# Kernel optimization log

Measured on AMD Instinct MI355X. Metric: run time of the kernel, lower is better.

Reference implementation:

```python
import jax, jax.numpy as jnp
import numpy as np

WINDOW = 60
DEPTH = 3
HIDDEN = 256
LN_EPS = 1e-5


def _lyndon_indices(d):
    # Lyndon words over alphabet {0..d-1}, lengths 2 and 3, lexicographic order
    # (signatory mode='words' extracts expanded-logsig coefficients at Lyndon words).
    i2 = np.array([(i, j) for i in range(d) for j in range(d) if (i, j) < (j, i)], dtype=np.int32)
    i3 = np.array([(i, j, k) for i in range(d) for j in range(d) for k in range(d)
                   if (i, j, k) < (j, k, i) and (i, j, k) < (k, i, j)], dtype=np.int32)
    return i2, i3


def _logsig_features(x):
    # x: [b, s, c] -> logsignature of time-augmented sliding windows: [b*s, sig_channels]
    b, s, c = x.shape
    d = c + 1
    # replicate-padded sliding windows via clipped gather (matches F.pad replicate + unfold)
    pos = jnp.clip(jnp.arange(s)[:, None] + jnp.arange(WINDOW)[None, :] - (WINDOW - 1), 0, s - 1)
    windows = x[:, pos, :]                                   # [b, s, W, c]
    t = jnp.linspace(0.0, 1.0, WINDOW, dtype=x.dtype)        # time augmentation channel
    t_b = jnp.broadcast_to(t[None, None, :, None], (b, s, WINDOW, 1))
    aug = jnp.concatenate([t_b, windows], axis=-1).reshape(b * s, WINDOW, d)
    N = b * s
    # basepoint=True: prepend zero point -> increments include the first point itself
    inc = jnp.diff(aug, axis=1, prepend=jnp.zeros((N, 1, d), aug.dtype))  # [N, W, d]
    inc_t = jnp.transpose(inc, (1, 0, 2))                    # [W, N, d]

    def chen_step(carry, v):
        S1, S2, S3 = carry
        vv = jnp.einsum('ni,nj->nij', v, v)
        vvv = jnp.einsum('nij,nk->nijk', vv, v)
        nS3 = S3 + jnp.einsum('nij,nk->nijk', S2, v) \
                 + 0.5 * jnp.einsum('ni,njk->nijk', S1, vv) + vvv / 6.0
        nS2 = S2 + jnp.einsum('ni,nj->nij', S1, v) + 0.5 * vv
        nS1 = S1 + v
        return (nS1, nS2, nS3), None

    init = (jnp.zeros((N, d), x.dtype), jnp.zeros((N, d, d), x.dtype), jnp.zeros((N, d, d, d), x.dtype))
    (S1, S2, S3), _ = jax.lax.scan(chen_step, init, inc_t)
    # log in truncated tensor algebra: log(1+x) = x - x^2/2 + x^3/3
    L1 = S1
    L2 = S2 - 0.5 * jnp.einsum('ni,nj->nij', S1, S1)
    L3 = (S3 - 0.5 * (jnp.einsum('ni,njk->nijk', S1, S2) + jnp.einsum('nij,nk->nijk', S2, S1))
          + jnp.einsum('ni,nj,nk->nijk', S1, S1, S1) / 3.0)
    i2, i3 = _lyndon_indices(d)
    f2 = L2[:, i2[:, 0], i2[:, 1]]
    f3 = L3[:, i3[:, 0], i3[:, 1], i3[:, 2]]
    return jnp.concatenate([L1, f2, f3], axis=-1)            # [N, sig_channels]


def setup_inputs() -> dict:
    key = jax.random.key(0)
    ks = jax.random.split(key, 5)
    b, s, c = 8, 2048, 8
    d = c + 1
    sig_channels = d + (d * d - d) // 2 + (d ** 3 - d) // 3  # 285 for d=9
    h2 = 2 * HIDDEN
    x = jax.random.normal(ks[0], (b, s, c), dtype=jnp.float32)
    w1 = jax.random.normal(ks[1], (sig_channels, h2), dtype=jnp.float32) / np.sqrt(sig_channels)
    b1 = jnp.zeros((h2,), jnp.float32)
    ln_g = jnp.ones((h2,), jnp.float32)
    ln_b = jnp.zeros((h2,), jnp.float32)
    w2 = jax.random.normal(ks[2], (h2, HIDDEN), dtype=jnp.float32) / np.sqrt(h2)
    b2 = jnp.zeros((HIDDEN,), jnp.float32)
    return {"x": x, "w1": w1, "b1": b1, "ln_g": ln_g, "ln_b": ln_b, "w2": w2, "b2": b2}


def reference(x, w1, b1, ln_g, ln_b, w2, b2):
    b, s, _ = x.shape
    feats = _logsig_features(x)                              # [b*s, sig_channels]
    h = jax.nn.gelu(feats @ w1 + b1, approximate=False)      # torch default GELU (erf)
    mu = jnp.mean(h, axis=-1, keepdims=True)
    var = jnp.var(h, axis=-1, keepdims=True)
    h = (h - mu) / jnp.sqrt(var + LN_EPS) * ln_g + ln_b      # LayerNorm; Dropout is eval no-op
    out = h @ w2 + b2
    return out.reshape(b, s, -1)
```

## Files before the change

kernel.cpp:

```cpp
#include <hip/hip_runtime.h>
#include <hip/hip_bf16.h>
#include <cstdint>
#include <cstddef>

typedef short short8 __attribute__((ext_vector_type(8)));
typedef float f32x4 __attribute__((ext_vector_type(4)));

#define NS    2048
#define KPAD  288
#define H2    512
#define HID   256
#define WPB   14
#define SBLK  147

__device__ __forceinline__ void gl2lds16(const void* g, void* l) {
    __builtin_amdgcn_global_load_lds(
        (const __attribute__((address_space(1))) void*)g,
        (__attribute__((address_space(3))) void*)l, 16, 0, 0);
}

__device__ __forceinline__ float geluf(float x) {
    return 0.5f * x * (1.0f + erff(x * 0.70710678118654752f));
}

__device__ __forceinline__ f32x4 shfl4(f32x4 v, int d) {
    f32x4 r;
    r[0] = __shfl_xor(v[0], d); r[1] = __shfl_xor(v[1], d);
    r[2] = __shfl_xor(v[2], d); r[3] = __shfl_xor(v[3], d);
    return r;
}

struct Tbl3 { short col[729]; };
static constexpr Tbl3 make_tbl3() {
    Tbl3 t{};
    for (int x = 0; x < 729; ++x) t.col[x] = -1;
    int r = 0;
    for (int i = 0; i < 9; ++i)
        for (int j = 0; j < 9; ++j)
            for (int k = 0; k < 9; ++k) {
                bool lt1 = (i < j) || (i == j && (j < k || (j == k && k < i)));
                bool lt2 = (i < k) || (i == k && (j < i || (j == i && k < j)));
                if (lt1 && lt2) { t.col[(i*9+j)*9+k] = (short)(45 + r); ++r; }
            }
    return t;
}
static constexpr Tbl3 TBL3 = make_tbl3();

#define SIG_DECLROW(a) \
    float S3_##a##_0=0.f,S3_##a##_1=0.f,S3_##a##_2=0.f,S3_##a##_3=0.f,S3_##a##_4=0.f, \
          S3_##a##_5=0.f,S3_##a##_6=0.f,S3_##a##_7=0.f,S3_##a##_8=0.f;
#define SIG_CHENROW(a) { const float ra = S2r##a + hh * v##a; \
    S3_##a##_0 += ra*v0; S3_##a##_1 += ra*v1; S3_##a##_2 += ra*v2; \
    S3_##a##_3 += ra*v3; S3_##a##_4 += ra*v4; S3_##a##_5 += ra*v5; \
    S3_##a##_6 += ra*v6; S3_##a##_7 += ra*v7; S3_##a##_8 += ra*v8; }
#define SIG_EMIT2(j2) if (ci < j2) { \
    const float val2 = S2r##j2 - 0.5f * S1i * s1v##j2; \
    const int col2 = 9 + ci*8 - (ci*(ci-1))/2 + (j2 - ci - 1); \
    frow[col2] = __float2bfloat16(val2); }
#define SIG_EMIT3(j3,k3) { const int col3 = TBL3.col[tb + j3*9 + k3]; \
    if (act && col3 >= 0) { \
        const float val3 = S3_##j3##_##k3 \
            - 0.5f * (S1i * S2w[j3*9+k3] + S2r##j3 * s1v##k3) \
            + S1i * s1v##j3 * s1v##k3 * (1.0f/3.0f); \
        frow[col3] = __float2bfloat16(val3); } }
#define SIG_EMIT3R(j3) SIG_EMIT3(j3,0) SIG_EMIT3(j3,1) SIG_EMIT3(j3,2) SIG_EMIT3(j3,3) \
    SIG_EMIT3(j3,4) SIG_EMIT3(j3,5) SIG_EMIT3(j3,6) SIG_EMIT3(j3,7) SIG_EMIT3(j3,8)

__global__ __launch_bounds__(128) __attribute__((amdgpu_waves_per_eu(1, 3)))
void sig_kernel(const float* __restrict__ x, __hip_bfloat16* __restrict__ feats) {
    __shared__ __align__(16) float X[73 * 8];
    __shared__ float S2buf[WPB * 81];
    __shared__ float S1buf[WPB * 9];

    const int blk = blockIdx.x;
    const int b   = blk / SBLK;
    const int s0  = (blk % SBLK) * WPB;
    const int lo  = (s0 - 59 > 0) ? (s0 - 59) : 0;
    const int hi  = (s0 + WPB - 1 < NS - 1) ? (s0 + WPB - 1) : (NS - 1);
    const int nrow = hi - lo + 1;
    const int tid = threadIdx.x;

    {
        const float4* src = (const float4*)(x + ((size_t)b * NS + lo) * 8);
        float4* dst = (float4*)X;
        const int n4 = nrow * 2;
        for (int t = tid; t < n4; t += 128) dst[t] = src[t];
    }
    __syncthreads();

    const int lane = tid & 63;
    const int wave = tid >> 6;
    const int wl   = lane / 9;
    const int ci   = lane - wl * 9;
    const int wl6  = (wl < 6) ? wl : 6;
    const int widx = wave * 7 + wl6;
    const int s    = s0 + widx;
    const bool act = (wl < 7) && (s < NS);

    SIG_DECLROW(0) SIG_DECLROW(1) SIG_DECLROW(2) SIG_DECLROW(3) SIG_DECLROW(4)
    SIG_DECLROW(5) SIG_DECLROW(6) SIG_DECLROW(7) SIG_DECLROW(8)
    float S2r0=0.f,S2r1=0.f,S2r2=0.f,S2r3=0.f,S2r4=0.f,S2r5=0.f,S2r6=0.f,S2r7=0.f,S2r8=0.f;
    float S1i = 0.f;
    float prev0=0.f,prev1=0.f,prev2=0.f,prev3=0.f,prev4=0.f,prev5=0.f,prev6=0.f,prev7=0.f;
    float pscal = 0.f;
    const int ioff = (ci > 0) ? (ci - 1) : 0;
    const int sm59 = s - 59;
    const float DT = 1.0f / 59.0f;

#pragma unroll 1
    for (int j = 0; j < 60; ++j) {
        int g = sm59 + j; g = (g > 0) ? g : 0;
        const float* row = &X[(g - lo) * 8];
        const float4 c0 = *(const float4*)(row);
        const float4 c1 = *(const float4*)(row + 4);
        const float rs  = row[ioff];
        const float dtj = (j == 0) ? 0.0f : DT;
        const float v0 = dtj;
        const float v1 = c0.x - prev0, v2 = c0.y - prev1, v3 = c0.z - prev2, v4 = c0.w - prev3;
        const float v5 = c1.x - prev4, v6 = c1.y - prev5, v7 = c1.z - prev6, v8 = c1.w - prev7;
        const float vi = (ci == 0) ? dtj : (rs - pscal);
        const float hh = 0.5f * S1i + vi * (1.0f / 6.0f);
        SIG_CHENROW(0) SIG_CHENROW(1) SIG_CHENROW(2) SIG_CHENROW(3) SIG_CHENROW(4)
        SIG_CHENROW(5) SIG_CHENROW(6) SIG_CHENROW(7) SIG_CHENROW(8)
        const float aa = S1i + 0.5f * vi;
        S2r0 += aa*v0; S2r1 += aa*v1; S2r2 += aa*v2; S2r3 += aa*v3; S2r4 += aa*v4;
        S2r5 += aa*v5; S2r6 += aa*v6; S2r7 += aa*v7; S2r8 += aa*v8;
        S1i += vi;
        prev0 = c0.x; prev1 = c0.y; prev2 = c0.z; prev3 = c0.w;
        prev4 = c1.x; prev5 = c1.y; prev6 = c1.z; prev7 = c1.w;
        pscal = rs;
    }

    if (wl < 7) {
        S1buf[widx * 9 + ci] = S1i;
        float* sb = &S2buf[widx * 81 + ci * 9];
        sb[0]=S2r0; sb[1]=S2r1; sb[2]=S2r2; sb[3]=S2r3; sb[4]=S2r4;
        sb[5]=S2r5; sb[6]=S2r6; sb[7]=S2r7; sb[8]=S2r8;
    }
    __syncthreads();

    const float* s1p = &S1buf[widx * 9];
    const float s1v0=s1p[0], s1v1=s1p[1], s1v2=s1p[2], s1v3=s1p[3], s1v4=s1p[4];
    const float s1v5=s1p[5], s1v6=s1p[6], s1v7=s1p[7], s1v8=s1p[8];
    const float* S2w = &S2buf[widx * 81];

    __hip_bfloat16* frow = feats + (size_t)(b * NS + (act ? s : 0)) * KPAD;
    if (act) {
        frow[ci] = __float2bfloat16(S1i);
        SIG_EMIT2(1) SIG_EMIT2(2) SIG_EMIT2(3) SIG_EMIT2(4)
        SIG_EMIT2(5) SIG_EMIT2(6) SIG_EMIT2(7) SIG_EMIT2(8)
        if (ci == 0) {
            frow[285] = __float2bfloat16(0.0f);
            frow[286] = __float2bfloat16(0.0f);
            frow[287] = __float2bfloat16(0.0f);
        }
    }
    const int tb = ci * 81;
    SIG_EMIT3R(0) SIG_EMIT3R(1) SIG_EMIT3R(2) SIG_EMIT3R(3) SIG_EMIT3R(4)
    SIG_EMIT3R(5) SIG_EMIT3R(6) SIG_EMIT3R(7) SIG_EMIT3R(8)
}

__global__ void convert_w1(const float* __restrict__ w1, __hip_bfloat16* __restrict__ w1T) {
    const int n = blockIdx.x;
    const int k = threadIdx.x;
    const float v = (k < 285) ? w1[(size_t)k * H2 + n] : 0.0f;
    w1T[(size_t)n * KPAD + k] = __float2bfloat16(v);
}
__global__ void convert_w2(const float* __restrict__ w2, __hip_bfloat16* __restrict__ w2T) {
    const int n = blockIdx.x;
    const int k = threadIdx.x;
    w2T[(size_t)n * H2 + k] = __float2bfloat16(w2[(size_t)k * HID + n]);
}

#define G1_DECLACC(m) f32x4 acc##m##0 = {0.f,0.f,0.f,0.f}, acc##m##1 = {0.f,0.f,0.f,0.f}, \
                            acc##m##2 = {0.f,0.f,0.f,0.f}, acc##m##3 = {0.f,0.f,0.f,0.f};
#define G1_MFMA(m) { const short8 afr = *(const short8*)(ldsA + ((m)*16 + l16)*32 + quad*8); \
    acc##m##0 = __builtin_amdgcn_mfma_f32_16x16x32_bf16(afr, bfrag0, acc##m##0, 0,0,0); \
    acc##m##1 = __builtin_amdgcn_mfma_f32_16x16x32_bf16(afr, bfrag1, acc##m##1, 0,0,0); \
    acc##m##2 = __builtin_amdgcn_mfma_f32_16x16x32_bf16(afr, bfrag2, acc##m##2, 0,0,0); \
    acc##m##3 = __builtin_amdgcn_mfma_f32_16x16x32_bf16(afr, bfrag3, acc##m##3, 0,0,0); }
#define G1_GELU1(m,n) { \
    acc##m##n[0]=geluf(acc##m##n[0]+bias##n); acc##m##n[1]=geluf(acc##m##n[1]+bias##n); \
    acc##m##n[2]=geluf(acc##m##n[2]+bias##n); acc##m##n[3]=geluf(acc##m##n[3]+bias##n); }
#define G1_GELUR(m) G1_GELU1(m,0) G1_GELU1(m,1) G1_GELU1(m,2) G1_GELU1(m,3)
#define G1_LNS(m) f32x4 psum##m = acc##m##0 + acc##m##1 + acc##m##2 + acc##m##3; \
    f32x4 psq##m = acc##m##0*acc##m##0 + acc##m##1*acc##m##1 + acc##m##2*acc##m##2 + acc##m##3*acc##m##3;
#define G1_STP(m) { const int rrp = (m)*16 + quad*4; \
    lnpart[wave][rrp+0][0]=psum##m[0]; lnpart[wave][rrp+0][1]=psq##m[0]; \
    lnpart[wave][rrp+1][0]=psum##m[1]; lnpart[wave][rrp+1][1]=psq##m[1]; \
    lnpart[wave][rrp+2][0]=psum##m[2]; lnpart[wave][rrp+2][1]=psq##m[2]; \
    lnpart[wave][rrp+3][0]=psum##m[3]; lnpart[wave][rrp+3][1]=psq##m[3]; }
#define G1_LDST(m) f32x4 mu##m; f32x4 rstd##m; { const int rrl = (m)*16 + quad*4; \
    mu##m[0]=lnstat[rrl+0][0]; mu##m[1]=lnstat[rrl+1][0]; mu##m[2]=lnstat[rrl+2][0]; mu##m[3]=lnstat[rrl+3][0]; \
    rstd##m[0]=lnstat[rrl+0][1]; rstd##m[1]=lnstat[rrl+1][1]; rstd##m[2]=lnstat[rrl+2][1]; rstd##m[3]=lnstat[rrl+3][1]; }
#define G1_OUT(m,n) { const int colo = wave*64 + (n)*16 + l16; \
    f32x4 hv = (acc##m##n - mu##m) * rstd##m * gv##n + bv##n; \
    const int rro = (m)*16 + quad*4; \
    hbuf[(size_t)(m0+rro+0)*H2 + colo] = __float2bfloat16(hv[0]); \
    hbuf[(size_t)(m0+rro+1)*H2 + colo] = __float2bfloat16(hv[1]); \
    hbuf[(size_t)(m0+rro+2)*H2 + colo] = __float2bfloat16(hv[2]); \
    hbuf[(size_t)(m0+rro+3)*H2 + colo] = __float2bfloat16(hv[3]); }
#define G1_OUTR(m) G1_OUT(m,0) G1_OUT(m,1) G1_OUT(m,2) G1_OUT(m,3)

__global__ __launch_bounds__(512) __attribute__((amdgpu_waves_per_eu(1, 3)))
void gemm1_kernel(
        const __hip_bfloat16* __restrict__ feats,
        const __hip_bfloat16* __restrict__ w1T,
        const float* __restrict__ b1,
        const float* __restrict__ lng,
        const float* __restrict__ lnb,
        __hip_bfloat16* __restrict__ hbuf) {
    __shared__ __align__(16) __hip_bfloat16 ldsA[64 * 32];
    __shared__ __align__(16) __hip_bfloat16 ldsB[512 * 32];
    __shared__ float lnpart[8][64][2];
    __shared__ float lnstat[64][2];

    const int tid  = threadIdx.x;
    const int wave = tid >> 6;
    const int lane = tid & 63;
    const int quad = lane >> 4;
    const int l16  = lane & 15;
    const int m0   = blockIdx.x * 64;

    G1_DECLACC(0) G1_DECLACC(1) G1_DECLACC(2) G1_DECLACC(3)

#pragma unroll 1
    for (int kt = 0; kt < 9; ++kt) {
        const int K0 = kt * 32;
        if (tid < 256) {
            const int m = tid >> 2, kc = tid & 3;
            gl2lds16(feats + (size_t)(m0 + m) * KPAD + K0 + kc * 8,
                     (char*)ldsA + (tid & ~63) * 16);
        }
#pragma unroll
        for (int q = 0; q < 4; ++q) {
            const int chunk = q * 512 + tid;
            const int n = chunk >> 2, kc = chunk & 3;
            gl2lds16(w1T + (size_t)n * KPAD + K0 + kc * 8,
                     (char*)ldsB + (chunk & ~63) * 16);
        }
        __syncthreads();
        const __hip_bfloat16* bbase = ldsB + (wave * 64 + l16) * 32 + quad * 8;
        const short8 bfrag0 = *(const short8*)(bbase);
        const short8 bfrag1 = *(const short8*)(bbase + 16 * 32);
        const short8 bfrag2 = *(const short8*)(bbase + 32 * 32);
        const short8 bfrag3 = *(const short8*)(bbase + 48 * 32);
        G1_MFMA(0) G1_MFMA(1) G1_MFMA(2) G1_MFMA(3)
        __syncthreads();
    }

    const float bias0 = b1[wave*64 +  0 + l16];
    const float bias1 = b1[wave*64 + 16 + l16];
    const float bias2 = b1[wave*64 + 32 + l16];
    const float bias3 = b1[wave*64 + 48 + l16];
    G1_GELUR(0) G1_GELUR(1) G1_GELUR(2) G1_GELUR(3)

    G1_LNS(0) G1_LNS(1) G1_LNS(2) G1_LNS(3)
#pragma unroll
    for (int d = 1; d < 16; d <<= 1) {
        psum0 += shfl4(psum0, d); psq0 += shfl4(psq0, d);
        psum1 += shfl4(psum1, d); psq1 += shfl4(psq1, d);
        psum2 += shfl4(psum2, d); psq2 += shfl4(psq2, d);
        psum3 += shfl4(psum3, d); psq3 += shfl4(psq3, d);
    }
    if (l16 == 0) { G1_STP(0) G1_STP(1) G1_STP(2) G1_STP(3) }
    __syncthreads();
    if (tid < 64) {
        float su = 0.f, sq = 0.f;
#pragma unroll
        for (int w = 0; w < 8; ++w) { su += lnpart[w][tid][0]; sq += lnpart[w][tid][1]; }
        const float mu  = su * (1.0f / 512.0f);
        const float var = sq * (1.0f / 512.0f) - mu * mu;
        lnstat[tid][0] = mu;
        lnstat[tid][1] = rsqrtf(var + 1e-5f);
    }
    __syncthreads();
    const float gv0 = lng[wave*64 +  0 + l16], bv0 = lnb[wave*64 +  0 + l16];
    const float gv1 = lng[wave*64 + 16 + l16], bv1 = lnb[wave*64 + 16 + l16];
    const float gv2 = lng[wave*64 + 32 + l16], bv2 = lnb[wave*64 + 32 + l16];
    const float gv3 = lng[wave*64 + 48 + l16], bv3 = lnb[wave*64 + 48 + l16];
    G1_LDST(0) G1_LDST(1) G1_LDST(2) G1_LDST(3)
    G1_OUTR(0) G1_OUTR(1) G1_OUTR(2) G1_OUTR(3)
}

#define G2_DECL(m) f32x4 bcc##m##0 = {0.f,0.f,0.f,0.f}, bcc##m##1 = {0.f,0.f,0.f,0.f};
#define G2_MFMA(m) { const short8 afr = *(const short8*)(ldsA + ((m)*16 + l16)*32 + quad*8); \
    bcc##m##0 = __builtin_amdgcn_mfma_f32_16x16x32_bf16(afr, bfr0, bcc##m##0, 0,0,0); \
    bcc##m##1 = __builtin_amdgcn_mfma_f32_16x16x32_bf16(afr, bfr1, bcc##m##1, 0,0,0); }
#define G2_OUT(m) { const int rro = (m)*16 + quad*4; \
    out[(size_t)(m0+rro+0)*HID + c0i] = bcc##m##0[0] + bb0; \
    out[(size_t)(m0+rro+1)*HID + c0i] = bcc##m##0[1] + bb0; \
    out[(size_t)(m0+rro+2)*HID + c0i] = bcc##m##0[2] + bb0; \
    out[(size_t)(m0+rro+3)*HID + c0i] = bcc##m##0[3] + bb0; \
    out[(size_t)(m0+rro+0)*HID + c1i] = bcc##m##1[0] + bb1; \
    out[(size_t)(m0+rro+1)*HID + c1i] = bcc##m##1[1] + bb1; \
    out[(size_t)(m0+rro+2)*HID + c1i] = bcc##m##1[2] + bb1; \
    out[(size_t)(m0+rro+3)*HID + c1i] = bcc##m##1[3] + bb1; }

__global__ __launch_bounds__(512) __attribute__((amdgpu_waves_per_eu(1, 3)))
void gemm2_kernel(
        const __hip_bfloat16* __restrict__ hbuf,
        const __hip_bfloat16* __restrict__ w2T,
        const float* __restrict__ b2,
        float* __restrict__ out) {
    __shared__ __align__(16) __hip_bfloat16 ldsA[64 * 32];
    __shared__ __align__(16) __hip_bfloat16 ldsB[256 * 32];
    const int tid  = threadIdx.x;
    const int wave = tid >> 6;
    const int lane = tid & 63;
    const int quad = lane >> 4;
    const int l16  = lane & 15;
    const int m0   = blockIdx.x * 64;

    G2_DECL(0) G2_DECL(1) G2_DECL(2) G2_DECL(3)

#pragma unroll 1
    for (int kt = 0; kt < 16; ++kt) {
        const int K0 = kt * 32;
        if (tid < 256) {
            const int m = tid >> 2, kc = tid & 3;
            gl2lds16(hbuf + (size_t)(m0 + m) * H2 + K0 + kc * 8,
                     (char*)ldsA + (tid & ~63) * 16);
        }
#pragma unroll
        for (int q = 0; q < 2; ++q) {
            const int chunk = q * 512 + tid;
            const int n = chunk >> 2, kc = chunk & 3;
            gl2lds16(w2T + (size_t)n * H2 + K0 + kc * 8,
                     (char*)ldsB + (chunk & ~63) * 16);
        }
        __syncthreads();
        const __hip_bfloat16* bbase = ldsB + (wave * 32 + l16) * 32 + quad * 8;
        const short8 bfr0 = *(const short8*)(bbase);
        const short8 bfr1 = *(const short8*)(bbase + 16 * 32);
        G2_MFMA(0) G2_MFMA(1) G2_MFMA(2) G2_MFMA(3)
        __syncthreads();
    }
    const float bb0 = b2[wave*32 +  0 + l16];
    const float bb1 = b2[wave*32 + 16 + l16];
    const int c0i = wave*32 +  0 + l16;
    const int c1i = wave*32 + 16 + l16;
    G2_OUT(0) G2_OUT(1) G2_OUT(2) G2_OUT(3)
}

extern "C" void kernel_launch(void* const* d_in, const int* in_sizes, int n_in,
                              void* d_out, int out_size, void* d_ws, size_t ws_size,
                              hipStream_t stream) {
    const float* x   = (const float*)d_in[0];
    const float* w1  = (const float*)d_in[1];
    const float* b1  = (const float*)d_in[2];
    const float* lng = (const float*)d_in[3];
    const float* lnb = (const float*)d_in[4];
    const float* w2  = (const float*)d_in[5];
    const float* b2  = (const float*)d_in[6];
    float* out = (float*)d_out;

    char* ws = (char*)d_ws;
    __hip_bfloat16* feats = (__hip_bfloat16*)(ws);
    __hip_bfloat16* hbuf  = (__hip_bfloat16*)(ws + 9437184);
    __hip_bfloat16* w1T   = (__hip_bfloat16*)(ws + 9437184 + 16777216);
    __hip_bfloat16* w2T   = (__hip_bfloat16*)(ws + 9437184 + 16777216 + 294912);

    convert_w1<<<dim3(512), dim3(288), 0, stream>>>(w1, w1T);
    convert_w2<<<dim3(256), dim3(512), 0, stream>>>(w2, w2T);
    sig_kernel<<<dim3(8 * SBLK), dim3(128), 0, stream>>>(x, feats);
    gemm1_kernel<<<dim3(16384 / 64), dim3(512), 0, stream>>>(feats, w1T, b1, lng, lnb, hbuf);
    gemm2_kernel<<<dim3(16384 / 64), dim3(512), 0, stream>>>(hbuf, w2T, b2, out);
}
```

Measured before the change: 175.8 us.

## Split signature S3 accumulation across three thread groups per window

Each (window, channel i) lane previously held all 81 S3 accumulators plus 9 S2 values. Now three 192-thread groups each own three rows of S2/S3, so per-thread state drops to 27+3 registers and the block grows to 576 threads covering 21 windows. The intent is to cut register pressure and raise occupancy and parallelism in the Chen recurrence. In exchange, every thread repeats the increment loads and S1 work, and the branch on group index must stay wave-uniform, which it does because 192 is a multiple of 64.

New measurement: 212.7 us. 21.0% more time.

```diff
diff --git a/kernel.cpp b/kernel.cpp
--- a/kernel.cpp
+++ b/kernel.cpp
@@ -10,8 +10,8 @@
 #define KPAD  288
 #define H2    512
 #define HID   256
-#define WPB   14
-#define SBLK  147
+#define WPB   21
+#define SBLK  98
 
 __device__ __forceinline__ void gl2lds16(const void* g, void* l) {
     __builtin_amdgcn_global_load_lds(
@@ -46,29 +46,74 @@
 }
 static constexpr Tbl3 TBL3 = make_tbl3();
 
-#define SIG_DECLROW(a) \
-    float S3_##a##_0=0.f,S3_##a##_1=0.f,S3_##a##_2=0.f,S3_##a##_3=0.f,S3_##a##_4=0.f, \
-          S3_##a##_5=0.f,S3_##a##_6=0.f,S3_##a##_7=0.f,S3_##a##_8=0.f;
-#define SIG_CHENROW(a) { const float ra = S2r##a + hh * v##a; \
-    S3_##a##_0 += ra*v0; S3_##a##_1 += ra*v1; S3_##a##_2 += ra*v2; \
-    S3_##a##_3 += ra*v3; S3_##a##_4 += ra*v4; S3_##a##_5 += ra*v5; \
-    S3_##a##_6 += ra*v6; S3_##a##_7 += ra*v7; S3_##a##_8 += ra*v8; }
-#define SIG_EMIT2(j2) if (ci < j2) { \
-    const float val2 = S2r##j2 - 0.5f * S1i * s1v##j2; \
-    const int col2 = 9 + ci*8 - (ci*(ci-1))/2 + (j2 - ci - 1); \
+#define SIG_LOOP(RA,RB,RC) \
+    for (int j = 0; j < 60; ++j) { \
+        int g = sm59 + j; g = (g > 0) ? g : 0; \
+        const float* row = &X[(g - lo) * 8]; \
+        const float4 c0 = *(const float4*)(row); \
+        const float4 c1 = *(const float4*)(row + 4); \
+        const float rs  = row[ioff]; \
+        const float dtj = (j == 0) ? 0.0f : DT; \
+        const float v0 = dtj; \
+        const float v1 = c0.x - prev0, v2 = c0.y - prev1, v3 = c0.z - prev2, v4 = c0.w - prev3; \
+        const float v5 = c1.x - prev4, v6 = c1.y - prev5, v7 = c1.z - prev6, v8 = c1.w - prev7; \
+        const float vi = (ci == 0) ? dtj : (rs - pscal); \
+        const float hh = 0.5f * S1i + vi * (1.0f / 6.0f); \
+        { const float ra = S2ra + hh * v##RA; \
+          S3a0 += ra*v0; S3a1 += ra*v1; S3a2 += ra*v2; S3a3 += ra*v3; S3a4 += ra*v4; \
+          S3a5 += ra*v5; S3a6 += ra*v6; S3a7 += ra*v7; S3a8 += ra*v8; } \
+        { const float rb = S2rb + hh * v##RB; \
+          S3b0 += rb*v0; S3b1 += rb*v1; S3b2 += rb*v2; S3b3 += rb*v3; S3b4 += rb*v4; \
+          S3b5 += rb*v5; S3b6 += rb*v6; S3b7 += rb*v7; S3b8 += rb*v8; } \
+        { const float rc = S2rc + hh * v##RC; \
+          S3c0 += rc*v0; S3c1 += rc*v1; S3c2 += rc*v2; S3c3 += rc*v3; S3c4 += rc*v4; \
+          S3c5 += rc*v5; S3c6 += rc*v6; S3c7 += rc*v7; S3c8 += rc*v8; } \
+        const float aa = S1i + 0.5f * vi; \
+        S2ra += aa * v##RA; S2rb += aa * v##RB; S2rc += aa * v##RC; \
+        S1i += vi; \
+        prev0 = c0.x; prev1 = c0.y; prev2 = c0.z; prev3 = c0.w; \
+        prev4 = c1.x; prev5 = c1.y; prev6 = c1.z; prev7 = c1.w; \
+        pscal = rs; \
+    }
+
+#define SIG_ST(RA,RB,RC) \
+    if (act) { \
+        if ((RA) == 0) S1buf[widx * 9 + ci] = S1i; \
+        float* sb = &S2buf[widx * 81 + ci * 9]; \
+        sb[RA] = S2ra; sb[RB] = S2rb; sb[RC] = S2rc; \
+    }
+
+#define SIG_E2(SL,J2) if (ci < (J2)) { \
+    const float val2 = S2r##SL - 0.5f * S1i * s1v##J2; \
+    const int col2 = 9 + ci*8 - (ci*(ci-1))/2 + ((J2) - ci - 1); \
     frow[col2] = __float2bfloat16(val2); }
-#define SIG_EMIT3(j3,k3) { const int col3 = TBL3.col[tb + j3*9 + k3]; \
-    if (act && col3 >= 0) { \
-        const float val3 = S3_##j3##_##k3 \
-            - 0.5f * (S1i * S2w[j3*9+k3] + S2r##j3 * s1v##k3) \
-            + S1i * s1v##j3 * s1v##k3 * (1.0f/3.0f); \
+
+#define SIG_E3(SL,R,K) { const int col3 = TBL3.col[tb + (R)*9 + (K)]; \
+    if (col3 >= 0) { \
+        const float val3 = S3##SL##K \
+            - 0.5f * (S1i * S2w[(R)*9+(K)] + S2r##SL * s1v##K) \
+            + S1i * s1v##R * s1v##K * (1.0f/3.0f); \
         frow[col3] = __float2bfloat16(val3); } }
-#define SIG_EMIT3R(j3) SIG_EMIT3(j3,0) SIG_EMIT3(j3,1) SIG_EMIT3(j3,2) SIG_EMIT3(j3,3) \
-    SIG_EMIT3(j3,4) SIG_EMIT3(j3,5) SIG_EMIT3(j3,6) SIG_EMIT3(j3,7) SIG_EMIT3(j3,8)
-
-__global__ __launch_bounds__(128) __attribute__((amdgpu_waves_per_eu(1, 3)))
+
+#define SIG_E3R(SL,R) SIG_E3(SL,R,0) SIG_E3(SL,R,1) SIG_E3(SL,R,2) SIG_E3(SL,R,3) \
+    SIG_E3(SL,R,4) SIG_E3(SL,R,5) SIG_E3(SL,R,6) SIG_E3(SL,R,7) SIG_E3(SL,R,8)
+
+#define SIG_EMIT(RA,RB,RC) \
+    if (act) { \
+        if ((RA) == 0) { \
+            frow[ci] = __float2bfloat16(S1i); \
+            if (ci == 0) { \
+                const __hip_bfloat16 z16 = __float2bfloat16(0.0f); \
+                frow[285] = z16; frow[286] = z16; frow[287] = z16; \
+            } \
+        } \
+        SIG_E2(a,RA) SIG_E2(b,RB) SIG_E2(c,RC) \
+        SIG_E3R(a,RA) SIG_E3R(b,RB) SIG_E3R(c,RC) \
+    }
+
+__global__ __launch_bounds__(576) __attribute__((amdgpu_waves_per_eu(1, 6)))
 void sig_kernel(const float* __restrict__ x, __hip_bfloat16* __restrict__ feats) {
-    __shared__ __align__(16) float X[73 * 8];
+    __shared__ __align__(16) float X[80 * 8];
     __shared__ float S2buf[WPB * 81];
     __shared__ float S1buf[WPB * 9];
 
@@ -84,22 +129,23 @@
         const float4* src = (const float4*)(x + ((size_t)b * NS + lo) * 8);
         float4* dst = (float4*)X;
         const int n4 = nrow * 2;
-        for (int t = tid; t < n4; t += 128) dst[t] = src[t];
+        for (int t = tid; t < n4; t += 576) dst[t] = src[t];
     }
     __syncthreads();
 
-    const int lane = tid & 63;
-    const int wave = tid >> 6;
-    const int wl   = lane / 9;
-    const int ci   = lane - wl * 9;
-    const int wl6  = (wl < 6) ? wl : 6;
-    const int widx = wave * 7 + wl6;
-    const int s    = s0 + widx;
-    const bool act = (wl < 7) && (s < NS);
-
-    SIG_DECLROW(0) SIG_DECLROW(1) SIG_DECLROW(2) SIG_DECLROW(3) SIG_DECLROW(4)
-    SIG_DECLROW(5) SIG_DECLROW(6) SIG_DECLROW(7) SIG_DECLROW(8)
-    float S2r0=0.f,S2r1=0.f,S2r2=0.f,S2r3=0.f,S2r4=0.f,S2r5=0.f,S2r6=0.f,S2r7=0.f,S2r8=0.f;
+    const int t3    = tid / 192;
+    const int lt    = tid - t3 * 192;
+    const int widx0 = lt / 9;
+    const int ci    = lt - widx0 * 9;
+    const int s_raw = s0 + widx0;
+    const bool act  = (lt < 189) && (s_raw < NS);
+    const int widx  = (widx0 < 20) ? widx0 : 20;
+    int s = s0 + widx; if (s > NS - 1) s = NS - 1;
+
+    float S3a0=0.f,S3a1=0.f,S3a2=0.f,S3a3=0.f,S3a4=0.f,S3a5=0.f,S3a6=0.f,S3a7=0.f,S3a8=0.f;
+    float S3b0=0.f,S3b1=0.f,S3b2=0.f,S3b3=0.f,S3b4=0.f,S3b5=0.f,S3b6=0.f,S3b7=0.f,S3b8=0.f;
+    float S3c0=0.f,S3c1=0.f,S3c2=0.f,S3c3=0.f,S3c4=0.f,S3c5=0.f,S3c6=0.f,S3c7=0.f,S3c8=0.f;
+    float S2ra=0.f, S2rb=0.f, S2rc=0.f;
     float S1i = 0.f;
     float prev0=0.f,prev1=0.f,prev2=0.f,prev3=0.f,prev4=0.f,prev5=0.f,prev6=0.f,prev7=0.f;
     float pscal = 0.f;
@@ -107,57 +153,25 @@
     const int sm59 = s - 59;
     const float DT = 1.0f / 59.0f;
 
-#pragma unroll 1
-    for (int j = 0; j < 60; ++j) {
-        int g = sm59 + j; g = (g > 0) ? g : 0;
-        const float* row = &X[(g - lo) * 8];
-        const float4 c0 = *(const float4*)(row);
-        const float4 c1 = *(const float4*)(row + 4);
-        const float rs  = row[ioff];
-        const float dtj = (j == 0) ? 0.0f : DT;
-        const float v0 = dtj;
-        const float v1 = c0.x - prev0, v2 = c0.y - prev1, v3 = c0.z - prev2, v4 = c0.w - prev3;
-        const float v5 = c1.x - prev4, v6 = c1.y - prev5, v7 = c1.z - prev6, v8 = c1.w - prev7;
-        const float vi = (ci == 0) ? dtj : (rs - pscal);
-        const float hh = 0.5f * S1i + vi * (1.0f / 6.0f);
-        SIG_CHENROW(0) SIG_CHENROW(1) SIG_CHENROW(2) SIG_CHENROW(3) SIG_CHENROW(4)
-        SIG_CHENROW(5) SIG_CHENROW(6) SIG_CHENROW(7) SIG_CHENROW(8)
-        const float aa = S1i + 0.5f * vi;
-        S2r0 += aa*v0; S2r1 += aa*v1; S2r2 += aa*v2; S2r3 += aa*v3; S2r4 += aa*v4;
-        S2r5 += aa*v5; S2r6 += aa*v6; S2r7 += aa*v7; S2r8 += aa*v8;
-        S1i += vi;
-        prev0 = c0.x; prev1 = c0.y; prev2 = c0.z; prev3 = c0.w;
-        prev4 = c1.x; prev5 = c1.y; prev6 = c1.z; prev7 = c1.w;
-        pscal = rs;
-    }
-
-    if (wl < 7) {
-        S1buf[widx * 9 + ci] = S1i;
-        float* sb = &S2buf[widx * 81 + ci * 9];
-        sb[0]=S2r0; sb[1]=S2r1; sb[2]=S2r2; sb[3]=S2r3; sb[4]=S2r4;
-        sb[5]=S2r5; sb[6]=S2r6; sb[7]=S2r7; sb[8]=S2r8;
-    }
+    if (t3 == 0)      { SIG_LOOP(0,1,2) }
+    else if (t3 == 1) { SIG_LOOP(3,4,5) }
+    else              { SIG_LOOP(6,7,8) }
+
+    if (t3 == 0)      { SIG_ST(0,1,2) }
+    else if (t3 == 1) { SIG_ST(3,4,5) }
+    else              { SIG_ST(6,7,8) }
     __syncthreads();
 
     const float* s1p = &S1buf[widx * 9];
     const float s1v0=s1p[0], s1v1=s1p[1], s1v2=s1p[2], s1v3=s1p[3], s1v4=s1p[4];
     const float s1v5=s1p[5], s1v6=s1p[6], s1v7=s1p[7], s1v8=s1p[8];
     const float* S2w = &S2buf[widx * 81];
-
-    __hip_bfloat16* frow = feats + (size_t)(b * NS + (act ? s : 0)) * KPAD;
-    if (act) {
-        frow[ci] = __float2bfloat16(S1i);
-        SIG_EMIT2(1) SIG_EMIT2(2) SIG_EMIT2(3) SIG_EMIT2(4)
-        SIG_EMIT2(5) SIG_EMIT2(6) SIG_EMIT2(7) SIG_EMIT2(8)
-        if (ci == 0) {
-            frow[285] = __float2bfloat16(0.0f);
-            frow[286] = __float2bfloat16(0.0f);
-            frow[287] = __float2bfloat16(0.0f);
-        }
-    }
     const int tb = ci * 81;
-    SIG_EMIT3R(0) SIG_EMIT3R(1) SIG_EMIT3R(2) SIG_EMIT3R(3) SIG_EMIT3R(4)
-    SIG_EMIT3R(5) SIG_EMIT3R(6) SIG_EMIT3R(7) SIG_EMIT3R(8)
+    __hip_bfloat16* frow = feats + (size_t)(b * NS + s) * KPAD;
+
+    if (t3 == 0)      { SIG_EMIT(0,1,2) }
+    else if (t3 == 1) { SIG_EMIT(3,4,5) }
+    else              { SIG_EMIT(6,7,8) }
 }
 
 __global__ void convert_w1(const float* __restrict__ w1, __hip_bfloat16* __restrict__ w1T) {
@@ -363,7 +377,7 @@
 
     convert_w1<<<dim3(512), dim3(288), 0, stream>>>(w1, w1T);
     convert_w2<<<dim3(256), dim3(512), 0, stream>>>(w2, w2T);
-    sig_kernel<<<dim3(8 * SBLK), dim3(128), 0, stream>>>(x, feats);
+    sig_kernel<<<dim3(8 * SBLK), dim3(576), 0, stream>>>(x, feats);
     gemm1_kernel<<<dim3(16384 / 64), dim3(512), 0, stream>>>(feats, w1T, b1, lng, lnb, hbuf);
     gemm2_kernel<<<dim3(16384 / 64), dim3(512), 0, stream>>>(hbuf, w2T, b2, out);
 }
```
